# Kernel tuning notes

Hardware: AMD Instinct MI355X
Metric: run time of the kernel (lower is better)

The kernel has to match this reference:

```python
import jax, jax.numpy as jnp
import numpy as np

N = 4096      # nodes
IN = 512      # in_dim
HID = 64      # hid_dim
OUT = 8       # out_dim (classes)
H = 2         # num_heads / meta-paths
SEM = 32      # semantic attention hidden size
P_EDGE = 0.005  # edge probability -> avg degree ~20


def setup_inputs() -> dict:
    key = jax.random.key(0)
    ks = jax.random.split(key, 12)
    h = jax.random.normal(ks[0], (N, IN), jnp.float32)
    # sparse binary adjacency per head, with self-loops (densified as in adj.to_dense())
    adj = (jax.random.uniform(ks[1], (H, N, N)) < P_EDGE).astype(jnp.float32)
    adj = jnp.clip(adj + jnp.eye(N, dtype=jnp.float32)[None], 0.0, 1.0)
    sc = lambda k, s: (jax.random.normal(k, s, jnp.float32) * 0.05)
    W1 = sc(ks[2], (H, IN, HID))
    b1 = jnp.zeros((H, HID), jnp.float32)
    Wq = sc(ks[3], (H, HID, HID)); bq = jnp.zeros((H, HID), jnp.float32)
    Wk = sc(ks[4], (H, HID, HID)); bk = jnp.zeros((H, HID), jnp.float32)
    Wv = sc(ks[5], (H, HID, HID)); bv = jnp.zeros((H, HID), jnp.float32)
    sem_W1 = sc(ks[6], (HID, SEM)); sem_b1 = jnp.zeros((SEM,), jnp.float32)
    sem_W2 = sc(ks[7], (SEM, 1))
    pred_W = sc(ks[8], (HID, OUT)); pred_b = jnp.zeros((OUT,), jnp.float32)
    return dict(h=h, adj=adj, W1=W1, b1=b1, Wq=Wq, bq=bq, Wk=Wk, bk=bk,
                Wv=Wv, bv=bv, sem_W1=sem_W1, sem_b1=sem_b1, sem_W2=sem_W2,
                pred_W=pred_W, pred_b=pred_b)


def reference(h, adj, W1, b1, Wq, bq, Wk, bk, Wv, bv,
              sem_W1, sem_b1, sem_W2, pred_W, pred_b):
    def embed(adj_i, W1_i, b1_i, Wq_i, bq_i, Wk_i, bk_i, Wv_i, bv_i):
        # GraphConvolution (Kipf): adj @ (h @ W) + b, then ReLU
        x = jax.nn.relu(adj_i @ (h @ W1_i) + b1_i)            # [N, HID]
        Q = x @ Wq_i + bq_i
        K = x @ Wk_i + bk_i
        V = x @ Wv_i + bv_i
        # dense-masked attention: adj.to_dense() * (Q K^T), softmax over rows
        A_tilde = adj_i * (Q @ K.T)                            # [N, N]
        att = jax.nn.softmax(A_tilde, axis=1)
        # gcn_norm: symmetric D^{-1/2} A D^{-1/2}, degree = row sums
        d = att.sum(axis=1)
        dinv = jnp.where(d > 0, jax.lax.rsqrt(d), 0.0)
        att_n = dinv[:, None] * att * dinv[None, :]
        return jax.nn.relu(att_n @ V)                          # [N, HID]

    z = jax.vmap(embed)(adj, W1, b1, Wq, bq, Wk, bk, Wv, bv)   # [H, N, HID]
    z = jnp.transpose(z, (1, 0, 2))                            # [N, H, HID]
    # SemanticAttention: project -> mean over nodes -> softmax over dim=1
    w = jnp.tanh(z @ sem_W1 + sem_b1) @ sem_W2                 # [N, H, 1]
    w = w.mean(axis=0)                                         # [H, 1]
    beta = jax.nn.softmax(w, axis=1)  # faithful to torch.softmax(w, dim=1)
    p2 = (beta[None] * z).sum(axis=1)                          # [N, HID]
    return jax.nn.softmax(p2 @ pred_W + pred_b, axis=1)        # [N, OUT]
```

## Files before the change

kernel.cpp:

```cpp
#include <hip/hip_runtime.h>
#include <hip/hip_bf16.h>

#define NN   4096
#define IND  512
#define HIDD 64
#define OUTD 8
#define NH   2
#define CAP  128

using bf16 = __hip_bfloat16;

__device__ __forceinline__ float b2f(bf16 v) { return __bfloat162float(v); }

__device__ __forceinline__ bool sniff_bf(const unsigned* __restrict__ adjw) {
    return (adjw[0] & 0xFFFFu) == 0x3F80u;
}
__device__ __forceinline__ float ldf(const void* p, int i, bool isbf) {
    return isbf ? b2f(((const bf16*)p)[i]) : ((const float*)p)[i];
}
__device__ __forceinline__ void load8f(const void* p, size_t off, bool isbf, float* o) {
    if (isbf) {
        uint4 d = *reinterpret_cast<const uint4*>((const bf16*)p + off);
        unsigned u[4] = {d.x, d.y, d.z, d.w};
#pragma unroll
        for (int w = 0; w < 4; ++w) {
            o[2 * w]     = __uint_as_float(u[w] << 16);
            o[2 * w + 1] = __uint_as_float(u[w] & 0xFFFF0000u);
        }
    } else {
        const float* q = (const float*)p + off;
        float4 a = *reinterpret_cast<const float4*>(q);
        float4 b = *reinterpret_cast<const float4*>(q + 4);
        o[0] = a.x; o[1] = a.y; o[2] = a.z; o[3] = a.w;
        o[4] = b.x; o[5] = b.y; o[6] = b.z; o[7] = b.w;
    }
}
__device__ __forceinline__ void load8_f32(const float* q, float* o) {
    float4 a = *reinterpret_cast<const float4*>(q);
    float4 b = *reinterpret_cast<const float4*>(q + 4);
    o[0] = a.x; o[1] = a.y; o[2] = a.z; o[3] = a.w;
    o[4] = b.x; o[5] = b.y; o[6] = b.z; o[7] = b.w;
}

__global__ void __launch_bounds__(256) k_csr(const void* __restrict__ adjv,
                                             int* __restrict__ deg,
                                             int* __restrict__ cols,
                                             float* __restrict__ vsum) {
    if (blockIdx.x == 0 && threadIdx.x < NH * HIDD) vsum[threadIdx.x] = 0.f;
    int row = blockIdx.x;
    __shared__ int cnt;
    __shared__ int lc[CAP];
    if (threadIdx.x == 0) cnt = 0;
    __syncthreads();
    if (sniff_bf((const unsigned*)adjv)) {
        const uint4* a4 = reinterpret_cast<const uint4*>((const bf16*)adjv + (size_t)row * NN);
#pragma unroll
        for (int it = 0; it < 2; ++it) {
            int v = threadIdx.x + it * 256;
            uint4 d = a4[v];
            unsigned u[4] = {d.x, d.y, d.z, d.w};
            int base = v * 8;
#pragma unroll
            for (int w = 0; w < 4; ++w) {
                if (u[w] & 0xFFFFu) { int p = atomicAdd(&cnt, 1); if (p < CAP) lc[p] = base + 2 * w; }
                if (u[w] >> 16)     { int p = atomicAdd(&cnt, 1); if (p < CAP) lc[p] = base + 2 * w + 1; }
            }
        }
    } else {
        const uint4* a4 = reinterpret_cast<const uint4*>((const float*)adjv + (size_t)row * NN);
#pragma unroll
        for (int it = 0; it < 4; ++it) {
            int v = threadIdx.x + it * 256;
            uint4 d = a4[v];
            unsigned u[4] = {d.x, d.y, d.z, d.w};
            int base = v * 4;
#pragma unroll
            for (int w = 0; w < 4; ++w) {
                if (u[w]) { int p = atomicAdd(&cnt, 1); if (p < CAP) lc[p] = base + w; }
            }
        }
    }
    __syncthreads();
    int c = cnt; if (c > CAP) c = CAP;
    if (threadIdx.x == 0) deg[row] = c;
    int* oc = cols + (size_t)row * CAP;
    for (int k = threadIdx.x; k < c; k += 256) oc[k] = lc[k];
}

template <typename T>
__device__ __forceinline__ void hw_body(const T* __restrict__ A,
                                        const T* __restrict__ B,
                                        float* __restrict__ C, int i0) {
    __shared__ __align__(16) float As[32][68];
    __shared__ __align__(16) float Bs[32][68];
    int tid = threadIdx.x;
    int r0 = (tid >> 4) * 4;
    int c0 = (tid & 15) * 4;
    float acc[4][4] = {};
    for (int kc = 0; kc < IND; kc += 32) {
        {
            int row = tid >> 2;
            int kp  = (tid & 3) * 8;
            float t8[8];
            load8f((const void*)A, (size_t)(i0 + row) * IND + kc + kp,
                   sizeof(T) == 2, t8);
#pragma unroll
            for (int j = 0; j < 8; ++j) As[kp + j][row] = t8[j];
        }
        {
            int kb = tid >> 3;
            int cp = (tid & 7) * 8;
            float t8[8];
            load8f((const void*)B, (size_t)(kc + kb) * HIDD + cp, sizeof(T) == 2, t8);
#pragma unroll
            for (int j = 0; j < 8; ++j) Bs[kb][cp + j] = t8[j];
        }
        __syncthreads();
#pragma unroll 8
        for (int k = 0; k < 32; ++k) {
            float4 av = *reinterpret_cast<const float4*>(&As[k][r0]);
            float4 bv = *reinterpret_cast<const float4*>(&Bs[k][c0]);
            float aa[4] = {av.x, av.y, av.z, av.w};
            float bb[4] = {bv.x, bv.y, bv.z, bv.w};
#pragma unroll
            for (int ia = 0; ia < 4; ++ia)
#pragma unroll
                for (int ib = 0; ib < 4; ++ib)
                    acc[ia][ib] = fmaf(aa[ia], bb[ib], acc[ia][ib]);
        }
        __syncthreads();
    }
#pragma unroll
    for (int ia = 0; ia < 4; ++ia)
        *reinterpret_cast<float4*>(C + (size_t)(i0 + r0 + ia) * HIDD + c0) =
            make_float4(acc[ia][0], acc[ia][1], acc[ia][2], acc[ia][3]);
}

__global__ void __launch_bounds__(256) k_hw(const void* __restrict__ h,
                                            const void* __restrict__ W1,
                                            const unsigned* __restrict__ adjw,
                                            float* __restrict__ hW) {
    int head = blockIdx.y;
    float* Ch = hW + (size_t)head * NN * HIDD;
    if (sniff_bf(adjw))
        hw_body<bf16>((const bf16*)h, (const bf16*)W1 + (size_t)head * IND * HIDD, Ch, blockIdx.x * 64);
    else
        hw_body<float>((const float*)h, (const float*)W1 + (size_t)head * IND * HIDD, Ch, blockIdx.x * 64);
}

__global__ void k_aggx(const float* __restrict__ hW, const void* __restrict__ b1,
                       const unsigned* __restrict__ adjw,
                       const int* __restrict__ deg, const int* __restrict__ cols,
                       float* __restrict__ x) {
    bool isbf = sniff_bf(adjw);
    int h = blockIdx.y;
    int i = blockIdx.x * 4 + threadIdx.y;
    int t = threadIdx.x;
    const float* hWh = hW + (size_t)h * NN * HIDD;
    int r = h * NN + i;
    int d = deg[r];
    const int* cl = cols + (size_t)r * CAP;
    float acc = ldf(b1, h * HIDD + t, isbf);
    for (int e = 0; e < d; ++e) acc += hWh[(size_t)cl[e] * HIDD + t];
    x[(size_t)r * HIDD + t] = fmaxf(acc, 0.f);
}

__global__ void __launch_bounds__(256) k_qkv(const float* __restrict__ x,
                                             const void* Wq, const void* bq,
                                             const void* Wk, const void* bk,
                                             const void* Wv, const void* bv,
                                             const unsigned* __restrict__ adjw,
                                             float* Q, float* K, float* V,
                                             float* __restrict__ vsum) {
    bool isbf = sniff_bf(adjw);
    int head = blockIdx.y, z = blockIdx.z;
    int i0 = blockIdx.x * 64;
    const void* W  = (z == 0) ? Wq : (z == 1) ? Wk : Wv;
    const void* bb = (z == 0) ? bq : (z == 1) ? bk : bv;
    float* C       = ((z == 0) ? Q : (z == 1) ? K : V) + (size_t)head * NN * HIDD;
    const float* xh = x + (size_t)head * NN * HIDD;

    __shared__ __align__(16) float As[64][68];
    __shared__ __align__(16) float Bs[64][68];
    int tid = threadIdx.x;
    {
        int row = tid >> 2;
        int kp  = (tid & 3) * 16;
        float t8[8];
        load8_f32(xh + (size_t)(i0 + row) * HIDD + kp, t8);
#pragma unroll
        for (int j = 0; j < 8; ++j) As[kp + j][row] = t8[j];
        load8_f32(xh + (size_t)(i0 + row) * HIDD + kp + 8, t8);
#pragma unroll
        for (int j = 0; j < 8; ++j) As[kp + 8 + j][row] = t8[j];
    }
    {
        int kb = tid >> 2;
        int cp = (tid & 3) * 16;
        size_t base = (size_t)head * HIDD * HIDD + (size_t)kb * HIDD + cp;
        float t8[8];
        load8f(W, base, isbf, t8);
#pragma unroll
        for (int j = 0; j < 8; ++j) Bs[kb][cp + j] = t8[j];
        load8f(W, base + 8, isbf, t8);
#pragma unroll
        for (int j = 0; j < 8; ++j) Bs[kb][cp + 8 + j] = t8[j];
    }
    __syncthreads();

    int r0 = (tid >> 4) * 4;
    int c0 = (tid & 15) * 4;
    float acc[4][4] = {};
#pragma unroll 8
    for (int k = 0; k < 64; ++k) {
        float4 av = *reinterpret_cast<const float4*>(&As[k][r0]);
        float4 bv4 = *reinterpret_cast<const float4*>(&Bs[k][c0]);
        float aa[4] = {av.x, av.y, av.z, av.w};
        float bbv[4] = {bv4.x, bv4.y, bv4.z, bv4.w};
#pragma unroll
        for (int ia = 0; ia < 4; ++ia)
#pragma unroll
            for (int ib = 0; ib < 4; ++ib)
                acc[ia][ib] = fmaf(aa[ia], bbv[ib], acc[ia][ib]);
    }
    float bz[4];
#pragma unroll
    for (int b = 0; b < 4; ++b) bz[b] = ldf(bb, head * HIDD + c0 + b, isbf);
#pragma unroll
    for (int ia = 0; ia < 4; ++ia)
        *reinterpret_cast<float4*>(C + (size_t)(i0 + r0 + ia) * HIDD + c0) =
            make_float4(acc[ia][0] + bz[0], acc[ia][1] + bz[1],
                        acc[ia][2] + bz[2], acc[ia][3] + bz[3]);

    if (z == 2) {
        float vpart[4];
#pragma unroll
        for (int ib = 0; ib < 4; ++ib)
            vpart[ib] = acc[0][ib] + acc[1][ib] + acc[2][ib] + acc[3][ib] + 64.f / 64.f * 0.f;
        __syncthreads();
        if (tid < HIDD) As[0][tid] = 0.f;
        __syncthreads();
#pragma unroll
        for (int ib = 0; ib < 4; ++ib)
            atomicAdd(&As[0][c0 + ib], vpart[ib] + 16.f * bz[ib]);
        __syncthreads();
        if (tid < HIDD) atomicAdd(&vsum[head * HIDD + tid], As[0][tid]);
    }
}

__global__ void __launch_bounds__(256) k_attn(const float* __restrict__ Q,
                                              const float* __restrict__ Km,
                                              const float* __restrict__ V,
                                              const float* __restrict__ vsum,
                                              const int* __restrict__ deg,
                                              const int* __restrict__ cols,
                                              const void* __restrict__ predW,
                                              const void* __restrict__ predb,
                                              const unsigned* __restrict__ adjw,
                                              void* __restrict__ outv) {
    bool isbf = sniff_bf(adjw);
    int wid = threadIdx.x >> 6;
    int t   = threadIdx.x & 63;
    int i   = blockIdx.x * 4 + wid;
    __shared__ __align__(16) float qs[4][64];
    __shared__ float wgt[4][CAP];
    __shared__ int   cs[4][CAP];
    __shared__ float p2s[4][64];
    float p2 = 0.f;

    for (int h = 0; h < NH; ++h) {
        int r = h * NN + i;
        int d = deg[r];
        const int* cl   = cols + (size_t)r * CAP;
        const float* Qh = Q + (size_t)h * NN * HIDD;
        const float* Kh = Km + (size_t)h * NN * HIDD;
        const float* Vh = V + (size_t)h * NN * HIDD;
        qs[wid][t] = Qh[(size_t)i * HIDD + t];
        for (int e = t; e < d; e += 64) cs[wid][e] = cl[e];

        float s0 = 0.f, s1 = 0.f;
        float lmax = 0.f;
        const float4* q4 = reinterpret_cast<const float4*>(qs[wid]);
        if (t < d) {
            const float4* K4 = reinterpret_cast<const float4*>(Kh + (size_t)cs[wid][t] * HIDD);
            float s = 0.f;
#pragma unroll 4
            for (int k = 0; k < 16; ++k) {
                float4 kv = K4[k]; float4 qv = q4[k];
                s += qv.x * kv.x + qv.y * kv.y + qv.z * kv.z + qv.w * kv.w;
            }
            s0 = s; lmax = fmaxf(lmax, s);
        }
        if (t + 64 < d) {
            const float4* K4 = reinterpret_cast<const float4*>(Kh + (size_t)cs[wid][t + 64] * HIDD);
            float s = 0.f;
#pragma unroll 4
            for (int k = 0; k < 16; ++k) {
                float4 kv = K4[k]; float4 qv = q4[k];
                s += qv.x * kv.x + qv.y * kv.y + qv.z * kv.z + qv.w * kv.w;
            }
            s1 = s; lmax = fmaxf(lmax, s);
        }
#pragma unroll
        for (int off = 32; off; off >>= 1) lmax = fmaxf(lmax, __shfl_xor(lmax, off));
        float m  = lmax;
        float eb = __expf(-m);
        float lsum = 0.f;
        if (t < d)      { float w = __expf(s0 - m); lsum += w; wgt[wid][t] = w - eb; }
        if (t + 64 < d) { float w = __expf(s1 - m); lsum += w; wgt[wid][t + 64] = w - eb; }
#pragma unroll
        for (int off = 32; off; off >>= 1) lsum += __shfl_xor(lsum, off);
        float Z = lsum + (float)(NN - d) * eb;
        float c = 1.f / Z;

        float acc = eb * vsum[h * HIDD + t];
        for (int e = 0; e < d; ++e) acc += wgt[wid][e] * Vh[(size_t)cs[wid][e] * HIDD + t];
        p2 += fmaxf(acc * c, 0.f);
    }

    p2s[wid][t] = p2;
    if (t < OUTD) {
        float a = ldf(predb, t, isbf);
#pragma unroll 8
        for (int k = 0; k < HIDD; ++k) a += p2s[wid][k] * ldf(predW, k * OUTD + t, isbf);
        float mx = a;
#pragma unroll
        for (int off = 4; off; off >>= 1) mx = fmaxf(mx, __shfl_xor(mx, off));
        float e = __expf(a - mx);
        float s = e;
#pragma unroll
        for (int off = 4; off; off >>= 1) s += __shfl_xor(s, off);
        float v = e / s;
        if (isbf) ((bf16*)outv)[(size_t)i * OUTD + t] = __float2bfloat16(v);
        else      ((float*)outv)[(size_t)i * OUTD + t] = v;
    }
}

extern "C" void kernel_launch(void* const* d_in, const int* in_sizes, int n_in,
                              void* d_out, int out_size, void* d_ws, size_t ws_size,
                              hipStream_t stream) {
    const void* adj = d_in[1];
    const unsigned* adjw = (const unsigned*)adj;

    char* w = (char*)d_ws;
    int*   deg  = (int*)w;                        w += (size_t)NH * NN * 4;
    int*   cols = (int*)w;                        w += (size_t)NH * NN * CAP * 4;
    float* hW   = (float*)w;                      w += (size_t)NH * NN * HIDD * 4;
    float* x    = (float*)w;                      w += (size_t)NH * NN * HIDD * 4;
    float* Q    = (float*)w;                      w += (size_t)NH * NN * HIDD * 4;
    float* K    = (float*)w;                      w += (size_t)NH * NN * HIDD * 4;
    float* V    = (float*)w;                      w += (size_t)NH * NN * HIDD * 4;
    float* vsum = (float*)w;                      w += (size_t)NH * HIDD * 4;

    k_csr <<<NH * NN, 256, 0, stream>>>(adj, deg, cols, vsum);
    k_hw  <<<dim3(NN / 64, NH), 256, 0, stream>>>(d_in[0], d_in[2], adjw, hW);
    k_aggx<<<dim3(NN / 4, NH), dim3(64, 4), 0, stream>>>(hW, d_in[3], adjw, deg, cols, x);
    k_qkv <<<dim3(NN / 64, NH, 3), 256, 0, stream>>>(x, d_in[4], d_in[5], d_in[6], d_in[7],
                                                     d_in[8], d_in[9], adjw, Q, K, V, vsum);
    k_attn<<<NN / 4, 256, 0, stream>>>(Q, K, V, vsum, deg, cols, d_in[13], d_in[14], adjw, d_out);
}
```

Measured before the change: 292.4 us.

## Fuse CSR build with hW GEMM and aggregation with QKV projection

Merges the adjacency-to-CSR scan and the h@W1 GEMM into one launch, with the first 128 blocks doing the GEMM and the rest scanning adjacency rows. It also fuses the neighbour aggregation (x) with the Q/K/V projections in a single kernel that keeps x in shared memory and computes all three outputs per block. This removes two launches and the x round-trip through global memory. In exchange it adds heavier per-block work and shared memory use in the fused QKV kernel, and the mixed-role first kernel may leave the two kinds of block unevenly balanced.

```diff
diff --git a/kernel.cpp b/kernel.cpp
--- a/kernel.cpp
+++ b/kernel.cpp
@@ -35,64 +35,12 @@
         o[4] = b.x; o[5] = b.y; o[6] = b.z; o[7] = b.w;
     }
 }
-__device__ __forceinline__ void load8_f32(const float* q, float* o) {
-    float4 a = *reinterpret_cast<const float4*>(q);
-    float4 b = *reinterpret_cast<const float4*>(q + 4);
-    o[0] = a.x; o[1] = a.y; o[2] = a.z; o[3] = a.w;
-    o[4] = b.x; o[5] = b.y; o[6] = b.z; o[7] = b.w;
-}
-
-__global__ void __launch_bounds__(256) k_csr(const void* __restrict__ adjv,
-                                             int* __restrict__ deg,
-                                             int* __restrict__ cols,
-                                             float* __restrict__ vsum) {
-    if (blockIdx.x == 0 && threadIdx.x < NH * HIDD) vsum[threadIdx.x] = 0.f;
-    int row = blockIdx.x;
-    __shared__ int cnt;
-    __shared__ int lc[CAP];
-    if (threadIdx.x == 0) cnt = 0;
-    __syncthreads();
-    if (sniff_bf((const unsigned*)adjv)) {
-        const uint4* a4 = reinterpret_cast<const uint4*>((const bf16*)adjv + (size_t)row * NN);
-#pragma unroll
-        for (int it = 0; it < 2; ++it) {
-            int v = threadIdx.x + it * 256;
-            uint4 d = a4[v];
-            unsigned u[4] = {d.x, d.y, d.z, d.w};
-            int base = v * 8;
-#pragma unroll
-            for (int w = 0; w < 4; ++w) {
-                if (u[w] & 0xFFFFu) { int p = atomicAdd(&cnt, 1); if (p < CAP) lc[p] = base + 2 * w; }
-                if (u[w] >> 16)     { int p = atomicAdd(&cnt, 1); if (p < CAP) lc[p] = base + 2 * w + 1; }
-            }
-        }
-    } else {
-        const uint4* a4 = reinterpret_cast<const uint4*>((const float*)adjv + (size_t)row * NN);
-#pragma unroll
-        for (int it = 0; it < 4; ++it) {
-            int v = threadIdx.x + it * 256;
-            uint4 d = a4[v];
-            unsigned u[4] = {d.x, d.y, d.z, d.w};
-            int base = v * 4;
-#pragma unroll
-            for (int w = 0; w < 4; ++w) {
-                if (u[w]) { int p = atomicAdd(&cnt, 1); if (p < CAP) lc[p] = base + w; }
-            }
-        }
-    }
-    __syncthreads();
-    int c = cnt; if (c > CAP) c = CAP;
-    if (threadIdx.x == 0) deg[row] = c;
-    int* oc = cols + (size_t)row * CAP;
-    for (int k = threadIdx.x; k < c; k += 256) oc[k] = lc[k];
-}
 
 template <typename T>
 __device__ __forceinline__ void hw_body(const T* __restrict__ A,
                                         const T* __restrict__ B,
-                                        float* __restrict__ C, int i0) {
-    __shared__ __align__(16) float As[32][68];
-    __shared__ __align__(16) float Bs[32][68];
+                                        float* __restrict__ C, int i0,
+                                        float (*As)[68], float (*Bs)[68]) {
     int tid = threadIdx.x;
     int r0 = (tid >> 4) * 4;
     int c0 = (tid & 15) * 4;
@@ -102,8 +50,7 @@
             int row = tid >> 2;
             int kp  = (tid & 3) * 8;
             float t8[8];
-            load8f((const void*)A, (size_t)(i0 + row) * IND + kc + kp,
-                   sizeof(T) == 2, t8);
+            load8f((const void*)A, (size_t)(i0 + row) * IND + kc + kp, sizeof(T) == 2, t8);
 #pragma unroll
             for (int j = 0; j < 8; ++j) As[kp + j][row] = t8[j];
         }
@@ -136,116 +83,157 @@
             make_float4(acc[ia][0], acc[ia][1], acc[ia][2], acc[ia][3]);
 }
 
-__global__ void __launch_bounds__(256) k_hw(const void* __restrict__ h,
-                                            const void* __restrict__ W1,
-                                            const unsigned* __restrict__ adjw,
-                                            float* __restrict__ hW) {
-    int head = blockIdx.y;
-    float* Ch = hW + (size_t)head * NN * HIDD;
-    if (sniff_bf(adjw))
-        hw_body<bf16>((const bf16*)h, (const bf16*)W1 + (size_t)head * IND * HIDD, Ch, blockIdx.x * 64);
-    else
-        hw_body<float>((const float*)h, (const float*)W1 + (size_t)head * IND * HIDD, Ch, blockIdx.x * 64);
-}
-
-__global__ void k_aggx(const float* __restrict__ hW, const void* __restrict__ b1,
-                       const unsigned* __restrict__ adjw,
-                       const int* __restrict__ deg, const int* __restrict__ cols,
-                       float* __restrict__ x) {
-    bool isbf = sniff_bf(adjw);
-    int h = blockIdx.y;
-    int i = blockIdx.x * 4 + threadIdx.y;
-    int t = threadIdx.x;
-    const float* hWh = hW + (size_t)h * NN * HIDD;
-    int r = h * NN + i;
-    int d = deg[r];
-    const int* cl = cols + (size_t)r * CAP;
-    float acc = ldf(b1, h * HIDD + t, isbf);
-    for (int e = 0; e < d; ++e) acc += hWh[(size_t)cl[e] * HIDD + t];
-    x[(size_t)r * HIDD + t] = fmaxf(acc, 0.f);
-}
-
-__global__ void __launch_bounds__(256) k_qkv(const float* __restrict__ x,
-                                             const void* Wq, const void* bq,
-                                             const void* Wk, const void* bk,
-                                             const void* Wv, const void* bv,
-                                             const unsigned* __restrict__ adjw,
-                                             float* Q, float* K, float* V,
-                                             float* __restrict__ vsum) {
-    bool isbf = sniff_bf(adjw);
-    int head = blockIdx.y, z = blockIdx.z;
-    int i0 = blockIdx.x * 64;
-    const void* W  = (z == 0) ? Wq : (z == 1) ? Wk : Wv;
-    const void* bb = (z == 0) ? bq : (z == 1) ? bk : bv;
-    float* C       = ((z == 0) ? Q : (z == 1) ? K : V) + (size_t)head * NN * HIDD;
-    const float* xh = x + (size_t)head * NN * HIDD;
-
-    __shared__ __align__(16) float As[64][68];
-    __shared__ __align__(16) float Bs[64][68];
+__global__ void __launch_bounds__(256) k1_csr_hw(const void* __restrict__ h,
+                                                 const void* __restrict__ W1,
+                                                 const void* __restrict__ adjv,
+                                                 int* __restrict__ deg,
+                                                 int* __restrict__ cols,
+                                                 float* __restrict__ hW,
+                                                 float* __restrict__ vsum) {
+    __shared__ __align__(16) float As[32][68];
+    __shared__ __align__(16) float Bs[32][68];
+    __shared__ int s_cnt;
+    __shared__ int s_lc[CAP];
+    bool isbf = sniff_bf((const unsigned*)adjv);
+    int bx = blockIdx.x;
+    if (bx < NH * (NN / 64)) {
+        if (bx == 0 && threadIdx.x < NH * HIDD) vsum[threadIdx.x] = 0.f;
+        int head = bx >> 6;
+        int i0 = (bx & 63) * 64;
+        float* Ch = hW + (size_t)head * NN * HIDD;
+        if (isbf)
+            hw_body<bf16>((const bf16*)h, (const bf16*)W1 + (size_t)head * IND * HIDD, Ch, i0, As, Bs);
+        else
+            hw_body<float>((const float*)h, (const float*)W1 + (size_t)head * IND * HIDD, Ch, i0, As, Bs);
+        return;
+    }
+    int row = bx - NH * (NN / 64);
+    if (threadIdx.x == 0) s_cnt = 0;
+    __syncthreads();
+    if (isbf) {
+        const uint4* a4 = reinterpret_cast<const uint4*>((const bf16*)adjv + (size_t)row * NN);
+#pragma unroll
+        for (int it = 0; it < 2; ++it) {
+            int v = threadIdx.x + it * 256;
+            uint4 d = a4[v];
+            unsigned u[4] = {d.x, d.y, d.z, d.w};
+            int base = v * 8;
+#pragma unroll
+            for (int w = 0; w < 4; ++w) {
+                if (u[w] & 0xFFFFu) { int p = atomicAdd(&s_cnt, 1); if (p < CAP) s_lc[p] = base + 2 * w; }
+                if (u[w] >> 16)     { int p = atomicAdd(&s_cnt, 1); if (p < CAP) s_lc[p] = base + 2 * w + 1; }
+            }
+        }
+    } else {
+        const uint4* a4 = reinterpret_cast<const uint4*>((const float*)adjv + (size_t)row * NN);
+#pragma unroll
+        for (int it = 0; it < 4; ++it) {
+            int v = threadIdx.x + it * 256;
+            uint4 d = a4[v];
+            unsigned u[4] = {d.x, d.y, d.z, d.w};
+            int base = v * 4;
+#pragma unroll
+            for (int w = 0; w < 4; ++w) {
+                if (u[w]) { int p = atomicAdd(&s_cnt, 1); if (p < CAP) s_lc[p] = base + w; }
+            }
+        }
+    }
+    __syncthreads();
+    int c = s_cnt; if (c > CAP) c = CAP;
+    if (threadIdx.x == 0) deg[row] = c;
+    int* oc = cols + (size_t)row * CAP;
+    for (int k = threadIdx.x; k < c; k += 256) oc[k] = s_lc[k];
+}
+
+__global__ void __launch_bounds__(256) k2_x_qkv(const float* __restrict__ hW,
+                                                const void* __restrict__ b1,
+                                                const void* Wq, const void* bq,
+                                                const void* Wk, const void* bk,
+                                                const void* Wv, const void* bv,
+                                                const void* __restrict__ adjv,
+                                                const int* __restrict__ deg,
+                                                const int* __restrict__ cols,
+                                                float* Q, float* K, float* V,
+                                                float* __restrict__ vsum) {
+    bool isbf = sniff_bf((const unsigned*)adjv);
+    int head = blockIdx.x >> 7;
+    int i0 = (blockIdx.x & 127) * 32;
+    __shared__ __align__(16) float xs[HIDD][36];
+    __shared__ __align__(16) float Ws[3][HIDD][68];
+    __shared__ float vred[HIDD];
     int tid = threadIdx.x;
-    {
-        int row = tid >> 2;
-        int kp  = (tid & 3) * 16;
-        float t8[8];
-        load8_f32(xh + (size_t)(i0 + row) * HIDD + kp, t8);
-#pragma unroll
-        for (int j = 0; j < 8; ++j) As[kp + j][row] = t8[j];
-        load8_f32(xh + (size_t)(i0 + row) * HIDD + kp + 8, t8);
-#pragma unroll
-        for (int j = 0; j < 8; ++j) As[kp + 8 + j][row] = t8[j];
+    int t  = tid & 63;
+    int wv = tid >> 6;
+    const float* hWh = hW + (size_t)head * NN * HIDD;
+
+    float bb1 = ldf(b1, head * HIDD + t, isbf);
+#pragma unroll
+    for (int rr = 0; rr < 8; ++rr) {
+        int n = i0 + rr * 4 + wv;
+        int r = head * NN + n;
+        int d = deg[r];
+        const int* cl = cols + (size_t)r * CAP;
+        float acc = bb1;
+        for (int e = 0; e < d; ++e) acc += hWh[(size_t)cl[e] * HIDD + t];
+        xs[t][rr * 4 + wv] = fmaxf(acc, 0.f);
     }
     {
         int kb = tid >> 2;
         int cp = (tid & 3) * 16;
-        size_t base = (size_t)head * HIDD * HIDD + (size_t)kb * HIDD + cp;
-        float t8[8];
-        load8f(W, base, isbf, t8);
-#pragma unroll
-        for (int j = 0; j < 8; ++j) Bs[kb][cp + j] = t8[j];
-        load8f(W, base + 8, isbf, t8);
-#pragma unroll
-        for (int j = 0; j < 8; ++j) Bs[kb][cp + 8 + j] = t8[j];
-    }
+        const void* Wz[3] = {Wq, Wk, Wv};
+#pragma unroll
+        for (int z = 0; z < 3; ++z) {
+            size_t base = (size_t)head * HIDD * HIDD + (size_t)kb * HIDD + cp;
+            float t8[8];
+            load8f(Wz[z], base, isbf, t8);
+#pragma unroll
+            for (int j = 0; j < 8; ++j) Ws[z][kb][cp + j] = t8[j];
+            load8f(Wz[z], base + 8, isbf, t8);
+#pragma unroll
+            for (int j = 0; j < 8; ++j) Ws[z][kb][cp + 8 + j] = t8[j];
+        }
+    }
+    if (tid < HIDD) vred[tid] = 0.f;
     __syncthreads();
 
-    int r0 = (tid >> 4) * 4;
+    int r0 = (tid >> 4) * 2;
     int c0 = (tid & 15) * 4;
-    float acc[4][4] = {};
-#pragma unroll 8
-    for (int k = 0; k < 64; ++k) {
-        float4 av = *reinterpret_cast<const float4*>(&As[k][r0]);
-        float4 bv4 = *reinterpret_cast<const float4*>(&Bs[k][c0]);
-        float aa[4] = {av.x, av.y, av.z, av.w};
-        float bbv[4] = {bv4.x, bv4.y, bv4.z, bv4.w};
-#pragma unroll
-        for (int ia = 0; ia < 4; ++ia)
-#pragma unroll
-            for (int ib = 0; ib < 4; ++ib)
-                acc[ia][ib] = fmaf(aa[ia], bbv[ib], acc[ia][ib]);
-    }
-    float bz[4];
-#pragma unroll
-    for (int b = 0; b < 4; ++b) bz[b] = ldf(bb, head * HIDD + c0 + b, isbf);
-#pragma unroll
-    for (int ia = 0; ia < 4; ++ia)
-        *reinterpret_cast<float4*>(C + (size_t)(i0 + r0 + ia) * HIDD + c0) =
-            make_float4(acc[ia][0] + bz[0], acc[ia][1] + bz[1],
-                        acc[ia][2] + bz[2], acc[ia][3] + bz[3]);
-
-    if (z == 2) {
-        float vpart[4];
-#pragma unroll
-        for (int ib = 0; ib < 4; ++ib)
-            vpart[ib] = acc[0][ib] + acc[1][ib] + acc[2][ib] + acc[3][ib] + 64.f / 64.f * 0.f;
-        __syncthreads();
-        if (tid < HIDD) As[0][tid] = 0.f;
-        __syncthreads();
-#pragma unroll
-        for (int ib = 0; ib < 4; ++ib)
-            atomicAdd(&As[0][c0 + ib], vpart[ib] + 16.f * bz[ib]);
-        __syncthreads();
-        if (tid < HIDD) atomicAdd(&vsum[head * HIDD + tid], As[0][tid]);
-    }
+    float acc[3][2][4] = {};
+#pragma unroll 4
+    for (int k = 0; k < HIDD; ++k) {
+        float a0 = xs[k][r0], a1 = xs[k][r0 + 1];
+#pragma unroll
+        for (int z = 0; z < 3; ++z) {
+            float4 w4 = *reinterpret_cast<const float4*>(&Ws[z][k][c0]);
+            float wb[4] = {w4.x, w4.y, w4.z, w4.w};
+#pragma unroll
+            for (int ib = 0; ib < 4; ++ib) {
+                acc[z][0][ib] = fmaf(a0, wb[ib], acc[z][0][ib]);
+                acc[z][1][ib] = fmaf(a1, wb[ib], acc[z][1][ib]);
+            }
+        }
+    }
+    const void* bz3[3] = {bq, bk, bv};
+    float* C3[3] = {Q + (size_t)head * NN * HIDD, K + (size_t)head * NN * HIDD,
+                    V + (size_t)head * NN * HIDD};
+    float bzv[4];
+#pragma unroll
+    for (int z = 0; z < 3; ++z) {
+#pragma unroll
+        for (int ib = 0; ib < 4; ++ib) bzv[ib] = ldf(bz3[z], head * HIDD + c0 + ib, isbf);
+#pragma unroll
+        for (int ia = 0; ia < 2; ++ia)
+            *reinterpret_cast<float4*>(C3[z] + (size_t)(i0 + r0 + ia) * HIDD + c0) =
+                make_float4(acc[z][ia][0] + bzv[0], acc[z][ia][1] + bzv[1],
+                            acc[z][ia][2] + bzv[2], acc[z][ia][3] + bzv[3]);
+    }
+#pragma unroll
+    for (int ib = 0; ib < 4; ++ib) bzv[ib] = ldf(bz3[2], head * HIDD + c0 + ib, isbf);
+#pragma unroll
+    for (int ib = 0; ib < 4; ++ib)
+        atomicAdd(&vred[c0 + ib], acc[2][0][ib] + acc[2][1][ib] + 2.f * bzv[ib]);
+    __syncthreads();
+    if (tid < HIDD) atomicAdd(&vsum[head * HIDD + tid], vred[tid]);
 }
 
 __global__ void __launch_bounds__(256) k_attn(const float* __restrict__ Q,
@@ -256,9 +244,9 @@
                                               const int* __restrict__ cols,
                                               const void* __restrict__ predW,
                                               const void* __restrict__ predb,
-                                              const unsigned* __restrict__ adjw,
+                                              const void* __restrict__ adjv,
                                               void* __restrict__ outv) {
-    bool isbf = sniff_bf(adjw);
+    bool isbf = sniff_bf((const unsigned*)adjv);
     int wid = threadIdx.x >> 6;
     int t   = threadIdx.x & 63;
     int i   = blockIdx.x * 4 + wid;
@@ -340,22 +328,21 @@
                               void* d_out, int out_size, void* d_ws, size_t ws_size,
                               hipStream_t stream) {
     const void* adj = d_in[1];
-    const unsigned* adjw = (const unsigned*)adj;
 
     char* w = (char*)d_ws;
     int*   deg  = (int*)w;                        w += (size_t)NH * NN * 4;
     int*   cols = (int*)w;                        w += (size_t)NH * NN * CAP * 4;
     float* hW   = (float*)w;                      w += (size_t)NH * NN * HIDD * 4;
-    float* x    = (float*)w;                      w += (size_t)NH * NN * HIDD * 4;
     float* Q    = (float*)w;                      w += (size_t)NH * NN * HIDD * 4;
     float* K    = (float*)w;                      w += (size_t)NH * NN * HIDD * 4;
     float* V    = (float*)w;                      w += (size_t)NH * NN * HIDD * 4;
     float* vsum = (float*)w;                      w += (size_t)NH * HIDD * 4;
 
-    k_csr <<<NH * NN, 256, 0, stream>>>(adj, deg, cols, vsum);
-    k_hw  <<<dim3(NN / 64, NH), 256, 0, stream>>>(d_in[0], d_in[2], adjw, hW);
-    k_aggx<<<dim3(NN / 4, NH), dim3(64, 4), 0, stream>>>(hW, d_in[3], adjw, deg, cols, x);
-    k_qkv <<<dim3(NN / 64, NH, 3), 256, 0, stream>>>(x, d_in[4], d_in[5], d_in[6], d_in[7],
-                                                     d_in[8], d_in[9], adjw, Q, K, V, vsum);
-    k_attn<<<NN / 4, 256, 0, stream>>>(Q, K, V, vsum, deg, cols, d_in[13], d_in[14], adjw, d_out);
-}
+    k1_csr_hw<<<NH * (NN / 64) + NH * NN, 256, 0, stream>>>(d_in[0], d_in[2], adj,
+                                                            deg, cols, hW, vsum);
+    k2_x_qkv <<<NH * (NN / 32), 256, 0, stream>>>(hW, d_in[3], d_in[4], d_in[5], d_in[6],
+                                                  d_in[7], d_in[8], d_in[9], adj,
+                                                  deg, cols, Q, K, V, vsum);
+    k_attn   <<<NN / 4, 256, 0, stream>>>(Q, K, V, vsum, deg, cols, d_in[13], d_in[14],
+                                          adj, d_out);
+}
```

Measured after the change: 306.8 us. 1.05x slower.
